# Optimization experiments

Measured on AMD Instinct MI355X. Metric: run time of the kernel, lower is better.

The kernel has to match this reference:

```python
import jax, jax.numpy as jnp
from jax import lax
import numpy as np

M_FILTERS = 128   # rows of responses D
N_CHANNELS = 1024 # cols of responses D (spectral channels)
BATCH = 4096
N_LAYERS = 17
IMAX = 50


def setup_inputs() -> dict:
    key = jax.random.key(0)
    k1, k2, k3, k4 = jax.random.split(key, 4)
    t1 = jax.random.normal(k1, (BATCH, N_CHANNELS), dtype=jnp.float32)
    t2 = jax.random.normal(k2, (BATCH, N_CHANNELS), dtype=jnp.float32)
    params = jax.random.uniform(k3, (M_FILTERS, N_LAYERS), dtype=jnp.float32)
    responses = jax.random.normal(k4, (M_FILTERS, N_CHANNELS), dtype=jnp.float32)
    return {
        "t1": t1,
        "t2": t2,
        "params": params,
        "thick_min": jnp.float32(0.0),
        "thick_max": jnp.float32(1.0),
        "beta_range": jnp.float32(0.1),
        "responses": responses,
    }


def _coherence_reduce(D0):
    """Faithful vectorized version of the 50-iteration coherence-reduction loop.

    The original per-row Python loop (Ri[i] > Rth branch) only reads row i and
    pre-computed Rth/delta, so it is exactly a masked row update.
    torch.linalg.eig on the symmetric matrices G is replaced by eigh (same
    eigenpairs up to sign/order; order is fixed by the explicit descending sort,
    and only the top-M eigenpairs reach the output D[:M,:]).
    """
    Mr, Nr = D0.shape
    ratio = jnp.float32(Nr / Mr)
    eye_b = jnp.eye(Nr, dtype=bool)

    def body(_, D):
        D = D / jnp.linalg.norm(D)                      # Frobenius norm over (0,1)
        G = D.T @ D                                     # [N, N]
        Sigma, V = jnp.linalg.eigh(G)
        Sigma = jnp.where(jnp.abs(Sigma) > 1e-10, ratio, Sigma)
        G = (V * Sigma[None, :]) @ V.T                  # V diag(Sigma) V^T
        G0 = jnp.abs(G - jnp.diag(jnp.diag(G)))
        Ri = jnp.sum(G0, axis=0)                        # [N]
        Rth = jnp.min(Ri)
        delta = Rth / (Nr - 1)
        mask = (Ri > Rth)[:, None]                      # rows to clip
        Gn = jnp.where(mask, delta * jnp.sign(G), G)
        Gn = jnp.where(eye_b, G, Gn)                    # keep original diagonal
        G = (Gn + Gn.T) * 0.5
        Sigma, V = jnp.linalg.eigh(G)
        order = jnp.argsort(-Sigma)                     # descending
        Sigma = Sigma[order]
        V = V[:, order]
        # Original: Sigma[M:-1]=0 then D = diag(Sigma)^{1/2} @ V.T, D = D[:M,:].
        # Only the top-M eigenpairs contribute to the first M rows.
        Dn = jnp.power(Sigma[:Mr], 0.5)[:, None] * V[:, :Mr].T  # [M, N]
        return Dn

    return lax.fori_loop(0, IMAX, body, D0)


def reference(t1, t2, params, thick_min, thick_max, beta_range, responses):
    # HybnetLoss: MSE match loss + hinge range loss (filter_loss is zeroed in source)
    match_loss = jnp.mean((t1 - t2) ** 2)
    d = jnp.float32(0.01)
    res = jnp.maximum((params - thick_min - d) / (-d),
                      (params - thick_max + d) / d)
    range_loss = jnp.mean(jnp.maximum(res, jnp.zeros_like(res)))
    original_loss = match_loss + beta_range * range_loss

    # HybnetLoss_plus: coherence-reduction regularizer on the response matrix
    D = _coherence_reduce(responses)
    rloss = jnp.mean((D - responses) ** 2)
    return original_loss + rloss
```

## Files before the change

kernel.cpp:

```cpp
#include <hip/hip_runtime.h>

#define NBLK 256

#define OFF_G    0
#define OFF_QT   1048576
#define OFF_YS   1179648
#define OFF_CS   1703936
#define OFF_LT   1835008
#define OFF_RP   1851392
#define OFF_ACC  1867776
#define OFF_BAR  1867792

#define BAR_A 0
#define BAR_B 32
#define BAR_C 64
#define BAR_D 72
#define BAR_E 73

typedef float v4f __attribute__((ext_vector_type(4)));

__device__ __forceinline__ void cld4_2(v4f& a, v4f& b,
                                       const float* pa, const float* pb) {
    asm volatile("global_load_dwordx4 %0, %2, off sc1\n\t"
                 "global_load_dwordx4 %1, %3, off sc1\n\t"
                 "s_waitcnt vmcnt(0)"
                 : "=&v"(a), "=&v"(b) : "v"(pa), "v"(pb) : "memory");
}
__device__ __forceinline__ void cld4_3(v4f& a, v4f& b, v4f& c,
                                       const float* pa, const float* pb,
                                       const float* pc) {
    asm volatile("global_load_dwordx4 %0, %3, off sc1\n\t"
                 "global_load_dwordx4 %1, %4, off sc1\n\t"
                 "global_load_dwordx4 %2, %5, off sc1\n\t"
                 "s_waitcnt vmcnt(0)"
                 : "=&v"(a), "=&v"(b), "=&v"(c)
                 : "v"(pa), "v"(pb), "v"(pc) : "memory");
}
__device__ __forceinline__ void cld4_4(v4f& a, v4f& b, v4f& c, v4f& d,
                                       const float* pa, const float* pb,
                                       const float* pc, const float* pd) {
    asm volatile("global_load_dwordx4 %0, %4, off sc1\n\t"
                 "global_load_dwordx4 %1, %5, off sc1\n\t"
                 "global_load_dwordx4 %2, %6, off sc1\n\t"
                 "global_load_dwordx4 %3, %7, off sc1\n\t"
                 "s_waitcnt vmcnt(0)"
                 : "=&v"(a), "=&v"(b), "=&v"(c), "=&v"(d)
                 : "v"(pa), "v"(pb), "v"(pc), "v"(pd) : "memory");
}
__device__ __forceinline__ void cld4_8(v4f& a, v4f& b, v4f& c, v4f& d,
                                       v4f& e, v4f& f, v4f& g, v4f& h,
                                       const float* pa, const float* pb,
                                       const float* pc, const float* pd,
                                       const float* pe, const float* pf,
                                       const float* pg, const float* ph) {
    asm volatile("global_load_dwordx4 %0, %8, off sc1\n\t"
                 "global_load_dwordx4 %1, %9, off sc1\n\t"
                 "global_load_dwordx4 %2, %10, off sc1\n\t"
                 "global_load_dwordx4 %3, %11, off sc1\n\t"
                 "global_load_dwordx4 %4, %12, off sc1\n\t"
                 "global_load_dwordx4 %5, %13, off sc1\n\t"
// ... 16 lines not shown
                 : "=&v"(a), "=&v"(b), "=&v"(c), "=&v"(d)
                 : "v"(pa), "v"(pb), "v"(pc), "v"(pd) : "memory");
}
__device__ __forceinline__ void cld1_8(float& a, float& b, float& c, float& d,
                                       float& e, float& f, float& g, float& h,
                                       const float* pa, const float* pb,
                                       const float* pc, const float* pd,
                                       const float* pe, const float* pf,
                                       const float* pg, const float* ph) {
    asm volatile("global_load_dword %0, %8, off sc1\n\t"
                 "global_load_dword %1, %9, off sc1\n\t"
                 "global_load_dword %2, %10, off sc1\n\t"
                 "global_load_dword %3, %11, off sc1\n\t"
                 "global_load_dword %4, %12, off sc1\n\t"
                 "global_load_dword %5, %13, off sc1\n\t"
                 "global_load_dword %6, %14, off sc1\n\t"
                 "global_load_dword %7, %15, off sc1\n\t"
                 "s_waitcnt vmcnt(0)"
                 : "=&v"(a), "=&v"(b), "=&v"(c), "=&v"(d),
                   "=&v"(e), "=&v"(f), "=&v"(g), "=&v"(h)
                 : "v"(pa), "v"(pb), "v"(pc), "v"(pd),
                   "v"(pe), "v"(pf), "v"(pg), "v"(ph) : "memory");
}

__device__ __forceinline__ void ast2(float* p, float a, float b) {
    union { unsigned long long u; float f[2]; } c; c.f[0] = a; c.f[1] = b;
    __hip_atomic_store((unsigned long long*)p, c.u,
                       __ATOMIC_RELAXED, __HIP_MEMORY_SCOPE_AGENT);
}
__device__ __forceinline__ float ald(const float* p) {
    return __hip_atomic_load(p, __ATOMIC_RELAXED, __HIP_MEMORY_SCOPE_AGENT);
}
__device__ __forceinline__ void ast(float* p, float x) {
    __hip_atomic_store(p, x, __ATOMIC_RELAXED, __HIP_MEMORY_SCOPE_AGENT);
}

__device__ __forceinline__ void bar_arrive(unsigned* bb, int line) {
    __syncthreads();
    if (threadIdx.x == 0)
        __hip_atomic_fetch_add(bb + line * 16, 1u,
                               __ATOMIC_RELAXED, __HIP_MEMORY_SCOPE_AGENT);
}
__device__ __forceinline__ void bar_wait(unsigned* bb, int wbase, int nlines,
                                         unsigned tgt) {
    if ((int)threadIdx.x < nlines) {
        while (__hip_atomic_load(bb + (wbase + threadIdx.x) * 16,
                                 __ATOMIC_RELAXED, __HIP_MEMORY_SCOPE_AGENT) < tgt)
            __builtin_amdgcn_s_sleep(2);
    }
    __builtin_amdgcn_s_waitcnt(0);
    __syncthreads();
}

union Smem {
    struct { float As[128][68]; float Bs[128][68]; } syrk;
    struct { float Cs[128][129]; float inv_d[16]; } chol;
    struct { float Ls[128 * 128]; float Xs[16][32]; } trsm;
    struct { float As[32][68]; float Bs[32][68]; float Rs[64][16]; } gg;
    struct { float Ri[1024]; float red[256]; float As[32][33]; float Bs[32][68]; } gy;
    float red[256];
};

__device__ __forceinline__ void dev_match(Smem* sm, const float* t1, const float* t2,
                                          float* accb, int w) {
    int tid = threadIdx.x;
    const float4* a = (const float4*)t1;
    const float4* b = (const float4*)t2;
    float s = 0.f;
    for (int i = w * 256 + tid; i < 1048576; i += 218 * 256) {
        float4 x = a[i], y = b[i];
        float d0 = x.x - y.x, d1 = x.y - y.y, d2 = x.z - y.z, d3 = x.w - y.w;
        s += d0 * d0 + d1 * d1 + d2 * d2 + d3 * d3;
    }
    sm->red[tid] = s; __syncthreads();
    for (int w2 = 128; w2 > 0; w2 >>= 1) {
        if (tid < w2) sm->red[tid] += sm->red[tid + w2];
        __syncthreads();
    }
    if (tid == 0) atomicAdd(&accb[0], sm->red[0]);
    __syncthreads();
}

// ... 11 lines not shown
    }
    sm->red[tid] = s; __syncthreads();
    for (int w = 128; w > 0; w >>= 1) {
        if (tid < w) sm->red[tid] += sm->red[tid + w];
        __syncthreads();
    }
    if (tid == 0) atomicAdd(&accb[1], sm->red[0]);
    __syncthreads();
}

__device__ __forceinline__ void dev_sumsq(Smem* sm, const float* X, float* accb, int w) {
    int tid = threadIdx.x;
    float s = 0.f;
    for (int i = w * 256 + tid; i < 131072; i += 1024) { float v = X[i]; s += v * v; }
    sm->red[tid] = s; __syncthreads();
    for (int w2 = 128; w2 > 0; w2 >>= 1) {
        if (tid < w2) sm->red[tid] += sm->red[tid + w2];
        __syncthreads();
    }
    if (tid == 0) atomicAdd(&accb[3], sm->red[0]);
    __syncthreads();
}

__device__ __forceinline__ void dev_syrk(Smem* sm, const float* A, int nsA,
                                         const float* B, int nsB, float* Cslab, int bid) {
    int tid = threadIdx.x;
    int q0 = (bid & 1) * 64, p0 = ((bid >> 1) & 1) * 64, z = bid >> 2;
    int kc = z * 128;
    if (nsA == 1) {
        for (int i = tid; i < 2048; i += 256) {
            int r = i >> 5, c4 = (i & 31) << 2;
            float4 v = *(const float4*)&A[(p0 + r) * 1024 + kc + c4];
            sm->syrk.As[c4][r] = v.x; sm->syrk.As[c4 + 1][r] = v.y;
            sm->syrk.As[c4 + 2][r] = v.z; sm->syrk.As[c4 + 3][r] = v.w;
        }
        for (int i = tid; i < 2048; i += 256) {
            int r = i >> 5, c4 = (i & 31) << 2;
            float4 v = *(const float4*)&B[(q0 + r) * 1024 + kc + c4];
            sm->syrk.Bs[c4][r] = v.x; sm->syrk.Bs[c4 + 1][r] = v.y;
            sm->syrk.Bs[c4 + 2][r] = v.z; sm->syrk.Bs[c4 + 3][r] = v.w;
        }
    } else {
        for (int cc = 0; cc < 8; cc += 2) {
            int i0 = tid + cc * 256, i1 = i0 + 256;
            int r0 = i0 >> 5, c40 = (i0 & 31) << 2;
            int r1 = i1 >> 5, c41 = (i1 & 31) << 2;
            const float* b0p = &A[(p0 + r0) * 1024 + kc + c40];
            const float* b1p = &A[(p0 + r1) * 1024 + kc + c41];
            v4f x0, x1, x2, x3, y0, y1, y2, y3;
            cld4_8(x0, x1, x2, x3, y0, y1, y2, y3,
                   b0p, b0p + 131072, b0p + 262144, b0p + 393216,
                   b1p, b1p + 131072, b1p + 262144, b1p + 393216);
            v4f s0 = x0; s0 += x1; s0 += x2; s0 += x3;
            v4f s1 = y0; s1 += y1; s1 += y2; s1 += y3;
            sm->syrk.As[c40][r0] = s0.x; sm->syrk.As[c40 + 1][r0] = s0.y;
            sm->syrk.As[c40 + 2][r0] = s0.z; sm->syrk.As[c40 + 3][r0] = s0.w;
            sm->syrk.As[c41][r1] = s1.x; sm->syrk.As[c41 + 1][r1] = s1.y;
            sm->syrk.As[c41 + 2][r1] = s1.z; sm->syrk.As[c41 + 3][r1] = s1.w;
        }
        for (int cc = 0; cc < 8; cc += 2) {
            int i0 = tid + cc * 256, i1 = i0 + 256;
            int r0 = i0 >> 5, c40 = (i0 & 31) << 2;
            int r1 = i1 >> 5, c41 = (i1 & 31) << 2;
            const float* b0p = &B[(q0 + r0) * 1024 + kc + c40];
            const float* b1p = &B[(q0 + r1) * 1024 + kc + c41];
            v4f x0, x1, x2, x3, y0, y1, y2, y3;
            cld4_8(x0, x1, x2, x3, y0, y1, y2, y3,
                   b0p, b0p + 131072, b0p + 262144, b0p + 393216,
                   b1p, b1p + 131072, b1p + 262144, b1p + 393216);
            v4f s0 = x0; s0 += x1; s0 += x2; s0 += x3;
            v4f s1 = y0; s1 += y1; s1 += y2; s1 += y3;
            sm->syrk.Bs[c40][r0] = s0.x; sm->syrk.Bs[c40 + 1][r0] = s0.y;
            sm->syrk.Bs[c40 + 2][r0] = s0.z; sm->syrk.Bs[c40 + 3][r0] = s0.w;
            sm->syrk.Bs[c41][r1] = s1.x; sm->syrk.Bs[c41 + 1][r1] = s1.y;
            sm->syrk.Bs[c41 + 2][r1] = s1.z; sm->syrk.Bs[c41 + 3][r1] = s1.w;
        }
    }
    __syncthreads();
    int tx = tid & 15, ty = tid >> 4;
    float acc[4][4] = {};
    for (int k = 0; k < 128; ++k) {
        float4 av = *(const float4*)&sm->syrk.As[k][ty * 4];
        float4 bv = *(const float4*)&sm->syrk.Bs[k][tx * 4];
        float a[4] = {av.x, av.y, av.z, av.w};
        float b[4] = {bv.x, bv.y, bv.z, bv.w};
        #pragma unroll
        for (int i = 0; i < 4; ++i)
            #pragma unroll
            for (int j = 0; j < 4; ++j) acc[i][j] += a[i] * b[j];
    }
    float* outp = &Cslab[z * 16384];
    for (int i = 0; i < 4; ++i) {
        float* op = &outp[(p0 + ty * 4 + i) * 128 + q0 + tx * 4];
        ast2(op, acc[i][0], acc[i][1]);
        ast2(op + 2, acc[i][2], acc[i][3]);
    }
    __syncthreads();
}

__device__ __forceinline__ void dev_chol(Smem* sm, const float* Cslab, float* Lt) {
    int tid = threadIdx.x;
    for (int cc = 0; cc < 16; ++cc) {
        int i = tid + cc * 256;
        int r = i >> 5, c4 = (i & 31) << 2;
        const float* b = &Cslab[i * 4];
        v4f z0, z1, z2, z3, z4, z5, z6, z7;
        cld4_8(z0, z1, z2, z3, z4, z5, z6, z7,
               b, b + 16384, b + 32768, b + 49152,
               b + 65536, b + 81920, b + 98304, b + 114688);
        v4f s = z0; s += z1; s += z2; s += z3; s += z4; s += z5; s += z6; s += z7;
        sm->chol.Cs[r][c4] = s.x; sm->chol.Cs[r][c4 + 1] = s.y;
        sm->chol.Cs[r][c4 + 2] = s.z; sm->chol.Cs[r][c4 + 3] = s.w;
    }
    __syncthreads();
    int lane = tid & 63;
    for (int kb = 0; kb < 8; ++kb) {
        int k0 = kb * 16;
        if (tid < 64) {
            float P0[16], P1[16], invs[16];
            #pragma unroll
            for (int u = 0; u < 16; ++u) {
                P0[u] = sm->chol.Cs[lane][k0 + u];
                P1[u] = sm->chol.Cs[lane + 64][k0 + u];
            }
            #pragma unroll
            for (int kk = 0; kk < 16; ++kk) {
                int k = k0 + kk;
                int src = k & 63;
                bool hi = (k >= 64);
                float pr[16];
                #pragma unroll
                for (int u = 0; u < 16; ++u)
                    if (u >= kk) pr[u] = __shfl(hi ? P1[u] : P0[u], src);
                float inv = 1.0f / pr[kk];
                invs[kk] = inv;
// ... 26 lines not shown
            if (has1) {
                #pragma unroll
                for (int u = 0; u < 16; ++u) w1[u] = sm->chol.Cs[j1][k0 + u] * sm->chol.inv_d[u];
            }
            if (has2) {
                #pragma unroll
                for (int u = 0; u < 16; ++u) w2[u] = sm->chol.Cs[j2][k0 + u] * sm->chol.inv_d[u];
            }
            int rlo = h * 32;
            int istart = rlo > base ? rlo : base;
            for (int i = istart; i < rlo + 32; ++i) {
                float v[16];
                #pragma unroll
                for (int u = 0; u < 16; ++u) v[u] = sm->chol.Cs[i][k0 + u];
                float a1 = 0.f, a2 = 0.f;
                #pragma unroll
                for (int u = 0; u < 16; ++u) { a1 += v[u] * w1[u]; a2 += v[u] * w2[u]; }
                if (has1) sm->chol.Cs[i][j1] -= a1;
                if (has2) sm->chol.Cs[i][j2] -= a2;
            }
        }
        __syncthreads();
    }
    for (int f2 = tid; f2 < 8192; f2 += 256) {
        int k = f2 >> 6, i2 = (f2 & 63) << 1;
        float d = sm->chol.Cs[k][k];
        float irs = 1.0f / sqrtf(d);
        float v0, v1;
        int i = i2;
        v0 = (i < k) ? 0.f : ((i == k) ? irs : sm->chol.Cs[i][k] * irs);
        i = i2 + 1;
        v1 = (i < k) ? 0.f : ((i == k) ? irs : sm->chol.Cs[i][k] * irs);
        ast2(&Lt[k * 128 + i2], v0, v1);
    }
    __syncthreads();
}

__device__ __forceinline__ void dev_trsm(Smem* sm, const float* Lt, const float* RHS,
                                         int ns, float* Qt, int bid) {
    int tid = threadIdx.x;
    int c = tid & 31, h = tid >> 5;
    int j0 = bid * 32;
    for (int cc = 0; cc < 16; cc += 4) {
        int i0 = tid + cc * 256, i1 = i0 + 256, i2 = i0 + 512, i3 = i0 + 768;
        v4f a, b, d, e;
        cld4_4(a, b, d, e, &Lt[i0 * 4], &Lt[i1 * 4], &Lt[i2 * 4], &Lt[i3 * 4]);
        *(v4f*)&sm->trsm.Ls[i0 * 4] = a;
        *(v4f*)&sm->trsm.Ls[i1 * 4] = b;
        *(v4f*)&sm->trsm.Ls[i2 * 4] = d;
        *(v4f*)&sm->trsm.Ls[i3 * 4] = e;
    }
    float acc[16];
    if (ns == 1) {
        #pragma unroll
        for (int r = 0; r < 16; ++r)
            acc[r] = RHS[(h * 16 + r) * 1024 + j0 + c];
    } else {
        for (int r = 0; r < 16; r += 2) {
            const float* p0 = &RHS[(h * 16 + r) * 1024 + j0 + c];
            const float* p1 = p0 + 1024;
            float a0, a1, a2, a3, b0, b1, b2, b3;
            cld1_8(a0, a1, a2, a3, b0, b1, b2, b3,
                   p0, p0 + 131072, p0 + 262144, p0 + 393216,
                   p1, p1 + 131072, p1 + 262144, p1 + 393216);
            acc[r] = ((a0 + a1) + a2) + a3;
            acc[r + 1] = ((b0 + b1) + b2) + b3;
        }
    }
    __syncthreads();
    float* Ls = sm->trsm.Ls;
    for (int pb = 0; pb < 8; ++pb) {
        int p0 = pb * 16;
        if (h == pb) {
            #pragma unroll
            for (int kk = 0; kk < 16; ++kk) {
                int k = p0 + kk;
                float x = acc[kk] * Ls[k * 128 + k];
                acc[kk] = x;
                sm->trsm.Xs[kk][c] = x;
                #pragma unroll
                for (int r = kk + 1; r < 16; ++r)
                    acc[r] -= Ls[k * 128 + p0 + r] * x;
            }
        }
        __syncthreads();
        if (h > pb) {
            int rb = h * 16;
            #pragma unroll
            for (int kk = 0; kk < 16; ++kk) {
                float x = sm->trsm.Xs[kk][c];
                const float4* lr = (const float4*)&Ls[(p0 + kk) * 128 + rb];
                #pragma unroll
                for (int g4 = 0; g4 < 4; ++g4) {
                    float4 lv = lr[g4];
                    acc[g4 * 4 + 0] -= lv.x * x;
                    acc[g4 * 4 + 1] -= lv.y * x;
                    acc[g4 * 4 + 2] -= lv.z * x;
                    acc[g4 * 4 + 3] -= lv.w * x;
                }
            }
        }
        __syncthreads();
    }
    #pragma unroll
    for (int r = 0; r < 16; ++r)
        ast(&Qt[(h * 16 + r) * 1024 + j0 + c], acc[r]);
}

__device__ __forceinline__ void dev_gemmG(Smem* sm, const float* Qt, float* G,
                                          float* Rpart, int bid) {
    int tid = threadIdx.x;
    int tx = tid & 15, ty = tid >> 4;
    int bx = bid & 15, by = bid >> 4;
    int a0 = by * 64, b0 = bx * 64;
    float acc[4][4] = {};
    for (int kc = 0; kc < 128; kc += 32) {
        int i0 = tid, i1 = tid + 256;
        int r0 = i0 >> 4, c40 = (i0 & 15) << 2;
        int r1 = i1 >> 4, c41 = (i1 & 15) << 2;
        v4f av0, av1, bv0, bv1;
        cld4_4(av0, av1, bv0, bv1,
               &Qt[(kc + r0) * 1024 + a0 + c40],
               &Qt[(kc + r1) * 1024 + a0 + c41],
               &Qt[(kc + r0) * 1024 + b0 + c40],
               &Qt[(kc + r1) * 1024 + b0 + c41]);
        *(v4f*)&sm->gg.As[r0][c40] = av0;
        *(v4f*)&sm->gg.As[r1][c41] = av1;
        *(v4f*)&sm->gg.Bs[r0][c40] = bv0;
        *(v4f*)&sm->gg.Bs[r1][c41] = bv1;
        __syncthreads();
        for (int k = 0; k < 32; ++k) {
            float4 av = *(const float4*)&sm->gg.As[k][ty * 4];
            float4 bv = *(const float4*)&sm->gg.Bs[k][tx * 4];
            float a[4] = {av.x, av.y, av.z, av.w};
            float b[4] = {bv.x, bv.y, bv.z, bv.w};
            #pragma unroll
            for (int i = 0; i < 4; ++i)
                #pragma unroll
                for (int j = 0; j < 4; ++j) acc[i][j] += a[i] * b[j];
        }
        __syncthreads();
    }
    float rsum[4] = {0.f, 0.f, 0.f, 0.f};
    for (int i = 0; i < 4; ++i) {
        int aa = a0 + ty * 4 + i;
        float g[4];
        #pragma unroll
        for (int j = 0; j < 4; ++j) g[j] = 8.f * acc[i][j];
        float* gp = &G[aa * 1024 + b0 + tx * 4];
        ast2(gp, g[0], g[1]);
        ast2(gp + 2, g[2], g[3]);
        int bb = b0 + tx * 4;
        #pragma unroll
// ... 27 lines not shown
        s0 += t3.x; s0 += t3.y; s0 += t3.z; s0 += t3.w;
        float s1 = 0.f;
        s1 += u0.x; s1 += u0.y; s1 += u0.z; s1 += u0.w;
        s1 += u1.x; s1 += u1.y; s1 += u1.z; s1 += u1.w;
        s1 += u2.x; s1 += u2.y; s1 += u2.z; s1 += u2.w;
        s1 += u3.x; s1 += u3.y; s1 += u3.z; s1 += u3.w;
        sm->gy.Ri[e0] = s0;
        sm->gy.Ri[e1] = s1;
        mn = fminf(mn, s0);
        mn = fminf(mn, s1);
    }
    sm->gy.red[tid] = mn;
    __syncthreads();
    for (int w = 128; w > 0; w >>= 1) {
        if (tid < w) sm->gy.red[tid] = fminf(sm->gy.red[tid], sm->gy.red[tid + w]);
        __syncthreads();
    }
    float r = sm->gy.red[0];
    *rth = r;
    *delta = r / 1023.f;
}

__device__ __forceinline__ void dev_gemmY(Smem* sm, const float* Qt, const float* G,
                                          float rth, float delta, float* Yslab, int bid) {
    int tid = threadIdx.x;
    int j0 = (bid & 15) * 64;
    int m0 = ((bid >> 4) & 3) * 32;
    int kz = bid >> 6;
    int kc0 = kz * 256;
    int tx = tid & 15, ty = tid >> 4;
    float acc[2][4] = {};
    for (int kc = kc0; kc < kc0 + 256; kc += 32) {
        int m = tid >> 3, k4 = (tid & 7) << 2;
        int iG0 = tid, iG1 = tid + 256;
        int rg0 = iG0 >> 4, cg0 = (iG0 & 15) << 2;
        int rg1 = iG1 >> 4, cg1 = (iG1 & 15) << 2;
        v4f q, g0, g1;
        cld4_3(q, g0, g1,
               &Qt[(m0 + m) * 1024 + kc + k4],
               &G[(kc + rg0) * 1024 + j0 + cg0],
               &G[(kc + rg1) * 1024 + j0 + cg1]);
        sm->gy.As[k4][m] = q.x;
        sm->gy.As[k4 + 1][m] = q.y;
        sm->gy.As[k4 + 2][m] = q.z;
        sm->gy.As[k4 + 3][m] = q.w;
        {
            int a = kc + rg0;
            float ria = sm->gy.Ri[a];
            #pragma unroll
            for (int u = 0; u < 4; ++u) {
                int b = j0 + cg0 + u;
                float g = g0[u];
                float sg = delta * ((g > 0.f) ? 1.f : ((g < 0.f) ? -1.f : 0.f));
                float ga = (ria > rth) ? sg : g;
                float gb = (sm->gy.Ri[b] > rth) ? sg : g;
                sm->gy.Bs[rg0][cg0 + u] = (a == b) ? g : 0.5f * (ga + gb);
            }
        }
        {
            int a = kc + rg1;
            float ria = sm->gy.Ri[a];
            #pragma unroll
            for (int u = 0; u < 4; ++u) {
                int b = j0 + cg1 + u;
                float g = g1[u];
                float sg = delta * ((g > 0.f) ? 1.f : ((g < 0.f) ? -1.f : 0.f));
                float ga = (ria > rth) ? sg : g;
                float gb = (sm->gy.Ri[b] > rth) ? sg : g;
                sm->gy.Bs[rg1][cg1 + u] = (a == b) ? g : 0.5f * (ga + gb);
            }
        }
        __syncthreads();
        for (int k = 0; k < 32; ++k) {
            float a0v = sm->gy.As[k][ty * 2], a1v = sm->gy.As[k][ty * 2 + 1];
            float4 bv = *(const float4*)&sm->gy.Bs[k][tx * 4];
            acc[0][0] += a0v * bv.x; acc[0][1] += a0v * bv.y;
            acc[0][2] += a0v * bv.z; acc[0][3] += a0v * bv.w;
            acc[1][0] += a1v * bv.x; acc[1][1] += a1v * bv.y;
            acc[1][2] += a1v * bv.z; acc[1][3] += a1v * bv.w;
        }
        __syncthreads();
    }
    float* outp = &Yslab[kz * 131072];
    for (int i = 0; i < 2; ++i) {
        float* op = &outp[(m0 + ty * 2 + i) * 1024 + j0 + tx * 4];
        ast2(op, acc[i][0], acc[i][1]);
        ast2(op + 2, acc[i][2], acc[i][3]);
    }
}

__device__ __forceinline__ void dev_trB(Smem* sm, const float* Qt, const float* G,
                                        const float* Rpart, float* accb, int bid) {
    int tid = threadIdx.x;
    float rth, delta;
    dev_ri(sm, Rpart, &rth, &delta);
    __syncthreads();
    int tx = tid & 15, ty = tid >> 4;
    int a0 = (bid >> 4) * 64, b0 = (bid & 15) * 64;
    float acc[4][4] = {};
    for (int kc = 0; kc < 128; kc += 32) {
        int i0 = tid, i1 = tid + 256;
        int r0 = i0 >> 4, c40 = (i0 & 15) << 2;
        int r1 = i1 >> 4, c41 = (i1 & 15) << 2;
        v4f av0, av1, bv0, bv1;
        cld4_4(av0, av1, bv0, bv1,
               &Qt[(kc + r0) * 1024 + a0 + c40],
               &Qt[(kc + r1) * 1024 + a0 + c41],
               &Qt[(kc + r0) * 1024 + b0 + c40],
               &Qt[(kc + r1) * 1024 + b0 + c41]);
        *(v4f*)&sm->syrk.As[r0][c40] = av0;
        *(v4f*)&sm->syrk.As[r1][c41] = av1;
        *(v4f*)&sm->syrk.Bs[r0][c40] = bv0;
        *(v4f*)&sm->syrk.Bs[r1][c41] = bv1;
        __syncthreads();
        for (int k = 0; k < 32; ++k) {
            float4 av = *(const float4*)&sm->syrk.As[k][ty * 4];
            float4 bv = *(const float4*)&sm->syrk.Bs[k][tx * 4];
            float a[4] = {av.x, av.y, av.z, av.w};
            float b[4] = {bv.x, bv.y, bv.z, bv.w};
            #pragma unroll
            for (int i = 0; i < 4; ++i)
                #pragma unroll
                for (int j = 0; j < 4; ++j) acc[i][j] += a[i] * b[j];
        }
        __syncthreads();
    }
    float rib[4];
    for (int j = 0; j < 4; ++j) {
        int bb = b0 + tx * 4 + j;
        v4f t0, t1, t2, t3;
        cld4_4(t0, t1, t2, t3, &Rpart[bb * 16], &Rpart[bb * 16 + 4],
               &Rpart[bb * 16 + 8], &Rpart[bb * 16 + 12]);
        float s = 0.f;
        s += t0.x; s += t0.y; s += t0.z; s += t0.w;
        s += t1.x; s += t1.y; s += t1.z; s += t1.w;
        s += t2.x; s += t2.y; s += t2.z; s += t2.w;
        s += t3.x; s += t3.y; s += t3.z; s += t3.w;
        rib[j] = s;
    }
    float s = 0.f;
// ... 2 lines not shown
        v4f t0, t1, t2, t3;
        cld4_4(t0, t1, t2, t3, &Rpart[aa * 16], &Rpart[aa * 16 + 4],
               &Rpart[aa * 16 + 8], &Rpart[aa * 16 + 12]);
        float ria = 0.f;
        ria += t0.x; ria += t0.y; ria += t0.z; ria += t0.w;
        ria += t1.x; ria += t1.y; ria += t1.z; ria += t1.w;
        ria += t2.x; ria += t2.y; ria += t2.z; ria += t2.w;
        ria += t3.x; ria += t3.y; ria += t3.z; ria += t3.w;
        float g0, g1, g2, g3;
        const float* gp = &G[aa * 1024 + b0 + tx * 4];
        cld1_4(g0, g1, g2, g3, gp, gp + 1, gp + 2, gp + 3);
        float gv[4] = {g0, g1, g2, g3};
        for (int j = 0; j < 4; ++j) {
            int bb = b0 + tx * 4 + j;
            float g = gv[j];
            float sg = delta * ((g > 0.f) ? 1.f : ((g < 0.f) ? -1.f : 0.f));
            float ga = (ria > rth) ? sg : g;
            float gb = (rib[j] > rth) ? sg : g;
            float gp2 = (aa == bb) ? g : 0.5f * (ga + gb);
            s += gp2 * acc[i][j];
        }
    }
    __syncthreads();
    sm->red[tid] = s;
    __syncthreads();
    for (int w = 128; w > 0; w >>= 1) {
        if (tid < w) sm->red[tid] += sm->red[tid + w];
        __syncthreads();
    }
    if (tid == 0) atomicAdd(&accb[2], sm->red[0]);
}

__global__ __launch_bounds__(256) void mega(const float* __restrict__ t1,
                                            const float* __restrict__ t2,
                                            const float* __restrict__ params,
                                            const float* __restrict__ tmin,
                                            const float* __restrict__ tmax,
                                            const float* __restrict__ beta,
                                            const float* __restrict__ R,
                                            float* ws, float* out) {
    float* G     = ws + OFF_G;
    float* Qt    = ws + OFF_QT;
    float* Yslab = ws + OFF_YS;
    float* Cslab = ws + OFF_CS;
    float* Lt    = ws + OFF_LT;
    float* Rpart = ws + OFF_RP;
    float* accb  = ws + OFF_ACC;
    unsigned* bb = (unsigned*)(ws + OFF_BAR);
    __shared__ Smem sm;
    int bid = blockIdx.x;
    unsigned phA = 0, phB = 0, phC = 0, phD = 0, phE = 0;

    if (bid < 32) dev_syrk(&sm, R, 1, R, 1, Cslab, bid);
    else if (bid < 250) dev_match(&sm, t1, t2, accb, bid - 32);
    else if (bid == 250) dev_range(&sm, params, tmin, tmax, accb);
    else if (bid < 255) dev_sumsq(&sm, R, accb, bid - 251);
    ++phC;
    if (bid < 32) bar_arrive(bb, BAR_C + (bid >> 2));
    if (bid == 0) { bar_wait(bb, BAR_C, 8, phC * 4); dev_chol(&sm, Cslab, Lt); }
    ++phD;
    if (bid == 0) bar_arrive(bb, BAR_D);
    if (bid < 32) { bar_wait(bb, BAR_D, 1, phD); dev_trsm(&sm, Lt, R, 1, Qt, bid); }
    ++phE;
    if (bid < 32) bar_arrive(bb, BAR_E + (bid >> 2));
    bar_wait(bb, BAR_E, 8, phE * 4);

    for (int it = 0; it < 50; ++it) {
        dev_gemmG(&sm, Qt, G, Rpart, bid);
        ++phA;
        bar_arrive(bb, BAR_A + (bid >> 3));
        bar_wait(bb, BAR_A, 32, phA * 8);
        {
            float rth, delta;
            dev_ri(&sm, Rpart, &rth, &delta);
            dev_gemmY(&sm, Qt, G, rth, delta, Yslab, bid);
        }
        ++phB;
        bar_arrive(bb, BAR_B + (bid >> 3));
        if (bid < 32) {
            bar_wait(bb, BAR_B, 32, phB * 8);
            dev_syrk(&sm, Yslab, 4, Yslab, 4, Cslab, bid);
        }
        ++phC;
        if (bid < 32) bar_arrive(bb, BAR_C + (bid >> 2));
        if (bid == 0) { bar_wait(bb, BAR_C, 8, phC * 4); dev_chol(&sm, Cslab, Lt); }
        ++phD;
        if (bid == 0) bar_arrive(bb, BAR_D);
        if (bid < 32) { bar_wait(bb, BAR_D, 1, phD); dev_trsm(&sm, Lt, Yslab, 4, Qt, bid); }
        ++phE;
        if (bid < 32) bar_arrive(bb, BAR_E + (bid >> 2));
        bar_wait(bb, BAR_E, 8, phE * 4);
    }

    dev_trB(&sm, Qt, G, Rpart, accb, bid);
    ++phA;
    bar_arrive(bb, BAR_A + (bid >> 3));
    if (bid == 0) {
        bar_wait(bb, BAR_A, 32, phA * 8);
        if (threadIdx.x == 0)
            out[0] = ald(&accb[0]) / 4194304.f + beta[0] * (ald(&accb[1]) / 2176.f)
                   + (ald(&accb[2]) + ald(&accb[3])) / 131072.f;
    }
}

extern "C" void kernel_launch(void* const* d_in, const int* in_sizes, int n_in,
                              void* d_out, int out_size, void* d_ws, size_t ws_size,
                              hipStream_t stream) {
    const float* t1 = (const float*)d_in[0];
    const float* t2 = (const float*)d_in[1];
    const float* params = (const float*)d_in[2];
    const float* tmin = (const float*)d_in[3];
    const float* tmax = (const float*)d_in[4];
    const float* beta = (const float*)d_in[5];
    const float* R = (const float*)d_in[6];
    float* ws = (float*)d_ws;
    float* out = (float*)d_out;

    hipMemsetAsync(ws + OFF_ACC, 0, 5312, stream);
    mega<<<NBLK, 256, 0, stream>>>(t1, t2, params, tmin, tmax, beta, R, ws, out);
}
```

Before: 8.408 ms.

## Fuse Cholesky with TRSM across blocks and use atomic accumulation instead of slabs

```diff
diff --git a/kernel.cpp b/kernel.cpp
--- a/kernel.cpp
+++ b/kernel.cpp
@@ -4,38 +4,19 @@
 
 #define OFF_G    0
 #define OFF_QT   1048576
-#define OFF_YS   1179648
-#define OFF_CS   1703936
-#define OFF_LT   1835008
+#define OFF_Y    1179648
+#define OFF_C    1703936
 #define OFF_RP   1851392
 #define OFF_ACC  1867776
 #define OFF_BAR  1867792
 
 #define BAR_A 0
-#define BAR_B 32
-#define BAR_C 64
-#define BAR_D 72
-#define BAR_E 73
+#define BAR_B 64
+#define BAR_C 128
+#define BAR_E 136
 
 typedef float v4f __attribute__((ext_vector_type(4)));
 
-__device__ __forceinline__ void cld4_2(v4f& a, v4f& b,
-                                       const float* pa, const float* pb) {
-    asm volatile("global_load_dwordx4 %0, %2, off sc1\n\t"
-                 "global_load_dwordx4 %1, %3, off sc1\n\t"
-                 "s_waitcnt vmcnt(0)"
-                 : "=&v"(a), "=&v"(b) : "v"(pa), "v"(pb) : "memory");
-}
-__device__ __forceinline__ void cld4_3(v4f& a, v4f& b, v4f& c,
-                                       const float* pa, const float* pb,
-                                       const float* pc) {
-    asm volatile("global_load_dwordx4 %0, %3, off sc1\n\t"
-                 "global_load_dwordx4 %1, %4, off sc1\n\t"
-                 "global_load_dwordx4 %2, %5, off sc1\n\t"
-                 "s_waitcnt vmcnt(0)"
-                 : "=&v"(a), "=&v"(b), "=&v"(c)
-                 : "v"(pa), "v"(pb), "v"(pc) : "memory");
-}
 __device__ __forceinline__ void cld4_4(v4f& a, v4f& b, v4f& c, v4f& d,
                                        const float* pa, const float* pb,
                                        const float* pc, const float* pd) {
@@ -98,6 +79,32 @@
                  : "v"(pa), "v"(pb), "v"(pc), "v"(pd),
                    "v"(pe), "v"(pf), "v"(pg), "v"(ph) : "memory");
 }
+__device__ __forceinline__ void iss4(v4f& a, v4f& b, v4f& c, v4f& d,
+                                     const float* pa, const float* pb,
+                                     const float* pc, const float* pd) {
+    asm volatile("global_load_dwordx4 %0, %4, off sc1\n\t"
+                 "global_load_dwordx4 %1, %5, off sc1\n\t"
+                 "global_load_dwordx4 %2, %6, off sc1\n\t"
+                 "global_load_dwordx4 %3, %7, off sc1"
+                 : "=&v"(a), "=&v"(b), "=&v"(c), "=&v"(d)
+                 : "v"(pa), "v"(pb), "v"(pc), "v"(pd) : "memory");
+}
+__device__ __forceinline__ void wt4(v4f& a, v4f& b, v4f& c, v4f& d) {
+    asm volatile("s_waitcnt vmcnt(0)"
+                 : "+v"(a), "+v"(b), "+v"(c), "+v"(d) :: "memory");
+}
+__device__ __forceinline__ void iss3(v4f& a, v4f& b, v4f& c,
+                                     const float* pa, const float* pb,
+                                     const float* pc) {
+    asm volatile("global_load_dwordx4 %0, %3, off sc1\n\t"
+                 "global_load_dwordx4 %1, %4, off sc1\n\t"
+                 "global_load_dwordx4 %2, %5, off sc1"
+                 : "=&v"(a), "=&v"(b), "=&v"(c)
+                 : "v"(pa), "v"(pb), "v"(pc) : "memory");
+}
+__device__ __forceinline__ void wt3(v4f& a, v4f& b, v4f& c) {
+    asm volatile("s_waitcnt vmcnt(0)" : "+v"(a), "+v"(b), "+v"(c) :: "memory");
+}
 
 __device__ __forceinline__ void ast2(float* p, float a, float b) {
     union { unsigned long long u; float f[2]; } c; c.f[0] = a; c.f[1] = b;
@@ -122,18 +129,18 @@
     if ((int)threadIdx.x < nlines) {
         while (__hip_atomic_load(bb + (wbase + threadIdx.x) * 16,
                                  __ATOMIC_RELAXED, __HIP_MEMORY_SCOPE_AGENT) < tgt)
-            __builtin_amdgcn_s_sleep(2);
+            __builtin_amdgcn_s_sleep(1);
     }
     __builtin_amdgcn_s_waitcnt(0);
     __syncthreads();
 }
 
 union Smem {
-    struct { float As[128][68]; float Bs[128][68]; } syrk;
-    struct { float Cs[128][129]; float inv_d[16]; } chol;
-    struct { float Ls[128 * 128]; float Xs[16][32]; } trsm;
     struct { float As[32][68]; float Bs[32][68]; float Rs[64][16]; } gg;
+    struct { float Cs[128][129]; float inv_d[16]; float irs[128];
+             float Xs[16][32]; } chol;
     struct { float Ri[1024]; float red[256]; float As[32][33]; float Bs[32][68]; } gy;
+    struct { float As[32][68]; float Bs[32][68]; float red[256]; } tb;
     float red[256];
 };
 
@@ -191,95 +198,76 @@
     __syncthreads();
 }
 
-__device__ __forceinline__ void dev_syrk(Smem* sm, const float* A, int nsA,
-                                         const float* B, int nsB, float* Cslab, int bid) {
+__device__ __forceinline__ void dev_syrk(Smem* sm, const float* A, const float* B,
+                                         float* C, int bid) {
     int tid = threadIdx.x;
     int q0 = (bid & 1) * 64, p0 = ((bid >> 1) & 1) * 64, z = bid >> 2;
-    int kc = z * 128;
-    if (nsA == 1) {
-        for (int i = tid; i < 2048; i += 256) {
-            int r = i >> 5, c4 = (i & 31) << 2;
-            float4 v = *(const float4*)&A[(p0 + r) * 1024 + kc + c4];
-            sm->syrk.As[c4][r] = v.x; sm->syrk.As[c4 + 1][r] = v.y;
-            sm->syrk.As[c4 + 2][r] = v.z; sm->syrk.As[c4 + 3][r] = v.w;
-        }
-        for (int i = tid; i < 2048; i += 256) {
-            int r = i >> 5, c4 = (i & 31) << 2;
-            float4 v = *(const float4*)&B[(q0 + r) * 1024 + kc + c4];
-            sm->syrk.Bs[c4][r] = v.x; sm->syrk.Bs[c4 + 1][r] = v.y;
-            sm->syrk.Bs[c4 + 2][r] = v.z; sm->syrk.Bs[c4 + 3][r] = v.w;
-        }
-    } else {
-        for (int cc = 0; cc < 8; cc += 2) {
-            int i0 = tid + cc * 256, i1 = i0 + 256;
-            int r0 = i0 >> 5, c40 = (i0 & 31) << 2;
-            int r1 = i1 >> 5, c41 = (i1 & 31) << 2;
-            const float* b0p = &A[(p0 + r0) * 1024 + kc + c40];
-            const float* b1p = &A[(p0 + r1) * 1024 + kc + c41];
-            v4f x0, x1, x2, x3, y0, y1, y2, y3;
-            cld4_8(x0, x1, x2, x3, y0, y1, y2, y3,
-                   b0p, b0p + 131072, b0p + 262144, b0p + 393216,
-                   b1p, b1p + 131072, b1p + 262144, b1p + 393216);
-            v4f s0 = x0; s0 += x1; s0 += x2; s0 += x3;
-            v4f s1 = y0; s1 += y1; s1 += y2; s1 += y3;
-            sm->syrk.As[c40][r0] = s0.x; sm->syrk.As[c40 + 1][r0] = s0.y;
-            sm->syrk.As[c40 + 2][r0] = s0.z; sm->syrk.As[c40 + 3][r0] = s0.w;
-            sm->syrk.As[c41][r1] = s1.x; sm->syrk.As[c41 + 1][r1] = s1.y;
-            sm->syrk.As[c41 + 2][r1] = s1.z; sm->syrk.As[c41 + 3][r1] = s1.w;
-        }
-        for (int cc = 0; cc < 8; cc += 2) {
-            int i0 = tid + cc * 256, i1 = i0 + 256;
-            int r0 = i0 >> 5, c40 = (i0 & 31) << 2;
-            int r1 = i1 >> 5, c41 = (i1 & 31) << 2;
-            const float* b0p = &B[(q0 + r0) * 1024 + kc + c40];
-            const float* b1p = &B[(q0 + r1) * 1024 + kc + c41];
-            v4f x0, x1, x2, x3, y0, y1, y2, y3;
-            cld4_8(x0, x1, x2, x3, y0, y1, y2, y3,
-                   b0p, b0p + 131072, b0p + 262144, b0p + 393216,
-                   b1p, b1p + 131072, b1p + 262144, b1p + 393216);
-            v4f s0 = x0; s0 += x1; s0 += x2; s0 += x3;
-            v4f s1 = y0; s1 += y1; s1 += y2; s1 += y3;
-            sm->syrk.Bs[c40][r0] = s0.x; sm->syrk.Bs[c40 + 1][r0] = s0.y;
-            sm->syrk.Bs[c40 + 2][r0] = s0.z; sm->syrk.Bs[c40 + 3][r0] = s0.w;
-            sm->syrk.Bs[c41][r1] = s1.x; sm->syrk.Bs[c41 + 1][r1] = s1.y;
-            sm->syrk.Bs[c41 + 2][r1] = s1.z; sm->syrk.Bs[c41 + 3][r1] = s1.w;
-        }
-    }
-    __syncthreads();
+    int kc0 = z * 128;
+    int p = tid & 63, kq = tid >> 6;
+    int kg = kq * 8;
     int tx = tid & 15, ty = tid >> 4;
     float acc[4][4] = {};
-    for (int k = 0; k < 128; ++k) {
-        float4 av = *(const float4*)&sm->syrk.As[k][ty * 4];
-        float4 bv = *(const float4*)&sm->syrk.Bs[k][tx * 4];
-        float a[4] = {av.x, av.y, av.z, av.w};
-        float b[4] = {bv.x, bv.y, bv.z, bv.w};
-        #pragma unroll
-        for (int i = 0; i < 4; ++i)
-            #pragma unroll
-            for (int j = 0; j < 4; ++j) acc[i][j] += a[i] * b[j];
-    }
-    float* outp = &Cslab[z * 16384];
-    for (int i = 0; i < 4; ++i) {
-        float* op = &outp[(p0 + ty * 4 + i) * 128 + q0 + tx * 4];
-        ast2(op, acc[i][0], acc[i][1]);
-        ast2(op + 2, acc[i][2], acc[i][3]);
-    }
-    __syncthreads();
-}
-
-__device__ __forceinline__ void dev_chol(Smem* sm, const float* Cslab, float* Lt) {
-    int tid = threadIdx.x;
-    for (int cc = 0; cc < 16; ++cc) {
-        int i = tid + cc * 256;
-        int r = i >> 5, c4 = (i & 31) << 2;
-        const float* b = &Cslab[i * 4];
+    v4f a0v, a1v, b0v, b1v;
+    {
+        const float* pa = &A[(p0 + p) * 1024 + kc0 + kg];
+        const float* pb = &B[(q0 + p) * 1024 + kc0 + kg];
+        iss4(a0v, a1v, b0v, b1v, pa, pa + 4, pb, pb + 4);
+    }
+    for (int ck = 0; ck < 4; ++ck) {
+        wt4(a0v, a1v, b0v, b1v);
+        __syncthreads();
+        sm->gg.As[kg + 0][p] = a0v.x; sm->gg.As[kg + 1][p] = a0v.y;
+        sm->gg.As[kg + 2][p] = a0v.z; sm->gg.As[kg + 3][p] = a0v.w;
+        sm->gg.As[kg + 4][p] = a1v.x; sm->gg.As[kg + 5][p] = a1v.y;
+        sm->gg.As[kg + 6][p] = a1v.z; sm->gg.As[kg + 7][p] = a1v.w;
+        sm->gg.Bs[kg + 0][p] = b0v.x; sm->gg.Bs[kg + 1][p] = b0v.y;
+        sm->gg.Bs[kg + 2][p] = b0v.z; sm->gg.Bs[kg + 3][p] = b0v.w;
+        sm->gg.Bs[kg + 4][p] = b1v.x; sm->gg.Bs[kg + 5][p] = b1v.y;
+        sm->gg.Bs[kg + 6][p] = b1v.z; sm->gg.Bs[kg + 7][p] = b1v.w;
+        __syncthreads();
+        if (ck < 3) {
+            const float* pa = &A[(p0 + p) * 1024 + kc0 + (ck + 1) * 32 + kg];
+            const float* pb = &B[(q0 + p) * 1024 + kc0 + (ck + 1) * 32 + kg];
+            iss4(a0v, a1v, b0v, b1v, pa, pa + 4, pb, pb + 4);
+        }
+        for (int k = 0; k < 32; ++k) {
+            float4 av = *(const float4*)&sm->gg.As[k][ty * 4];
+            float4 bv = *(const float4*)&sm->gg.Bs[k][tx * 4];
+            float a[4] = {av.x, av.y, av.z, av.w};
+            float b[4] = {bv.x, bv.y, bv.z, bv.w};
+            #pragma unroll
+            for (int i = 0; i < 4; ++i)
+                #pragma unroll
+                for (int j = 0; j < 4; ++j) acc[i][j] += a[i] * b[j];
+        }
+        __syncthreads();
+    }
+    for (int i = 0; i < 4; ++i)
+        for (int j = 0; j < 4; ++j)
+            atomicAdd(&C[(p0 + ty * 4 + i) * 128 + q0 + tx * 4 + j], acc[i][j]);
+}
+
+__device__ __forceinline__ void dev_cholTrsm(Smem* sm, const float* C, const float* RHS,
+                                             float* Qt, int bid) {
+    int tid = threadIdx.x;
+    {
+        const float* base = C + tid * 64;
         v4f z0, z1, z2, z3, z4, z5, z6, z7;
         cld4_8(z0, z1, z2, z3, z4, z5, z6, z7,
-               b, b + 16384, b + 32768, b + 49152,
-               b + 65536, b + 81920, b + 98304, b + 114688);
-        v4f s = z0; s += z1; s += z2; s += z3; s += z4; s += z5; s += z6; s += z7;
-        sm->chol.Cs[r][c4] = s.x; sm->chol.Cs[r][c4 + 1] = s.y;
-        sm->chol.Cs[r][c4 + 2] = s.z; sm->chol.Cs[r][c4 + 3] = s.w;
+               base, base + 4, base + 8, base + 12,
+               base + 16, base + 20, base + 24, base + 28);
+        int r = tid >> 1, c0 = (tid & 1) * 64;
+        *(v4f*)&sm->chol.Cs[r][c0]      = z0; *(v4f*)&sm->chol.Cs[r][c0 + 4]  = z1;
+        *(v4f*)&sm->chol.Cs[r][c0 + 8]  = z2; *(v4f*)&sm->chol.Cs[r][c0 + 12] = z3;
+        *(v4f*)&sm->chol.Cs[r][c0 + 16] = z4; *(v4f*)&sm->chol.Cs[r][c0 + 20] = z5;
+        *(v4f*)&sm->chol.Cs[r][c0 + 24] = z6; *(v4f*)&sm->chol.Cs[r][c0 + 28] = z7;
+        cld4_8(z0, z1, z2, z3, z4, z5, z6, z7,
+               base + 32, base + 36, base + 40, base + 44,
+               base + 48, base + 52, base + 56, base + 60);
+        *(v4f*)&sm->chol.Cs[r][c0 + 32] = z0; *(v4f*)&sm->chol.Cs[r][c0 + 36] = z1;
+        *(v4f*)&sm->chol.Cs[r][c0 + 40] = z2; *(v4f*)&sm->chol.Cs[r][c0 + 44] = z3;
+        *(v4f*)&sm->chol.Cs[r][c0 + 48] = z4; *(v4f*)&sm->chol.Cs[r][c0 + 52] = z5;
+        *(v4f*)&sm->chol.Cs[r][c0 + 56] = z6; *(v4f*)&sm->chol.Cs[r][c0 + 60] = z7;
     }
     __syncthreads();
     int lane = tid & 63;
@@ -352,65 +340,33 @@
         }
         __syncthreads();
     }
-    for (int f2 = tid; f2 < 8192; f2 += 256) {
-        int k = f2 >> 6, i2 = (f2 & 63) << 1;
-        float d = sm->chol.Cs[k][k];
-        float irs = 1.0f / sqrtf(d);
-        float v0, v1;
-        int i = i2;
-        v0 = (i < k) ? 0.f : ((i == k) ? irs : sm->chol.Cs[i][k] * irs);
-        i = i2 + 1;
-        v1 = (i < k) ? 0.f : ((i == k) ? irs : sm->chol.Cs[i][k] * irs);
-        ast2(&Lt[k * 128 + i2], v0, v1);
-    }
-    __syncthreads();
-}
-
-__device__ __forceinline__ void dev_trsm(Smem* sm, const float* Lt, const float* RHS,
-                                         int ns, float* Qt, int bid) {
-    int tid = threadIdx.x;
+    if (tid < 128) sm->chol.irs[tid] = 1.0f / sqrtf(sm->chol.Cs[tid][tid]);
     int c = tid & 31, h = tid >> 5;
     int j0 = bid * 32;
-    for (int cc = 0; cc < 16; cc += 4) {
-        int i0 = tid + cc * 256, i1 = i0 + 256, i2 = i0 + 512, i3 = i0 + 768;
-        v4f a, b, d, e;
-        cld4_4(a, b, d, e, &Lt[i0 * 4], &Lt[i1 * 4], &Lt[i2 * 4], &Lt[i3 * 4]);
-        *(v4f*)&sm->trsm.Ls[i0 * 4] = a;
-        *(v4f*)&sm->trsm.Ls[i1 * 4] = b;
-        *(v4f*)&sm->trsm.Ls[i2 * 4] = d;
-        *(v4f*)&sm->trsm.Ls[i3 * 4] = e;
-    }
     float acc[16];
-    if (ns == 1) {
-        #pragma unroll
-        for (int r = 0; r < 16; ++r)
-            acc[r] = RHS[(h * 16 + r) * 1024 + j0 + c];
-    } else {
-        for (int r = 0; r < 16; r += 2) {
-            const float* p0 = &RHS[(h * 16 + r) * 1024 + j0 + c];
-            const float* p1 = p0 + 1024;
-            float a0, a1, a2, a3, b0, b1, b2, b3;
-            cld1_8(a0, a1, a2, a3, b0, b1, b2, b3,
-                   p0, p0 + 131072, p0 + 262144, p0 + 393216,
-                   p1, p1 + 131072, p1 + 262144, p1 + 393216);
-            acc[r] = ((a0 + a1) + a2) + a3;
-            acc[r + 1] = ((b0 + b1) + b2) + b3;
-        }
-    }
-    __syncthreads();
-    float* Ls = sm->trsm.Ls;
+    {
+        const float* p = &RHS[(h * 16) * 1024 + j0 + c];
+        cld1_8(acc[0], acc[1], acc[2], acc[3], acc[4], acc[5], acc[6], acc[7],
+               p, p + 1024, p + 2048, p + 3072, p + 4096, p + 5120, p + 6144, p + 7168);
+        cld1_8(acc[8], acc[9], acc[10], acc[11], acc[12], acc[13], acc[14], acc[15],
+               p + 8192, p + 9216, p + 10240, p + 11264,
+               p + 12288, p + 13312, p + 14336, p + 15360);
+    }
+    __syncthreads();
     for (int pb = 0; pb < 8; ++pb) {
         int p0 = pb * 16;
         if (h == pb) {
             #pragma unroll
             for (int kk = 0; kk < 16; ++kk) {
                 int k = p0 + kk;
-                float x = acc[kk] * Ls[k * 128 + k];
+                float irsk = sm->chol.irs[k];
+                float x = acc[kk] * irsk;
                 acc[kk] = x;
-                sm->trsm.Xs[kk][c] = x;
+                sm->chol.Xs[kk][c] = x;
+                float xs = x * irsk;
                 #pragma unroll
                 for (int r = kk + 1; r < 16; ++r)
-                    acc[r] -= Ls[k * 128 + p0 + r] * x;
+                    acc[r] -= sm->chol.Cs[p0 + r][k] * xs;
             }
         }
         __syncthreads();
@@ -418,16 +374,11 @@
             int rb = h * 16;
             #pragma unroll
             for (int kk = 0; kk < 16; ++kk) {
-                float x = sm->trsm.Xs[kk][c];
-                const float4* lr = (const float4*)&Ls[(p0 + kk) * 128 + rb];
-                #pragma unroll
-                for (int g4 = 0; g4 < 4; ++g4) {
-                    float4 lv = lr[g4];
-                    acc[g4 * 4 + 0] -= lv.x * x;
-                    acc[g4 * 4 + 1] -= lv.y * x;
-                    acc[g4 * 4 + 2] -= lv.z * x;
-                    acc[g4 * 4 + 3] -= lv.w * x;
-                }
+                int k = p0 + kk;
+                float xs = sm->chol.Xs[kk][c] * sm->chol.irs[k];
+                #pragma unroll
+                for (int r = 0; r < 16; ++r)
+                    acc[r] -= sm->chol.Cs[rb + r][k] * xs;
             }
         }
         __syncthreads();
@@ -443,22 +394,27 @@
     int tx = tid & 15, ty = tid >> 4;
     int bx = bid & 15, by = bid >> 4;
     int a0 = by * 64, b0 = bx * 64;
+    int r0 = tid >> 4, c4 = (tid & 15) << 2;
+    int r1 = 16 + r0;
     float acc[4][4] = {};
+    v4f av0, av1, bv0, bv1;
+    iss4(av0, av1, bv0, bv1,
+         &Qt[r0 * 1024 + a0 + c4], &Qt[r1 * 1024 + a0 + c4],
+         &Qt[r0 * 1024 + b0 + c4], &Qt[r1 * 1024 + b0 + c4]);
     for (int kc = 0; kc < 128; kc += 32) {
-        int i0 = tid, i1 = tid + 256;
-        int r0 = i0 >> 4, c40 = (i0 & 15) << 2;
-        int r1 = i1 >> 4, c41 = (i1 & 15) << 2;
-        v4f av0, av1, bv0, bv1;
-        cld4_4(av0, av1, bv0, bv1,
-               &Qt[(kc + r0) * 1024 + a0 + c40],
-               &Qt[(kc + r1) * 1024 + a0 + c41],
-               &Qt[(kc + r0) * 1024 + b0 + c40],
-               &Qt[(kc + r1) * 1024 + b0 + c41]);
-        *(v4f*)&sm->gg.As[r0][c40] = av0;
-        *(v4f*)&sm->gg.As[r1][c41] = av1;
-        *(v4f*)&sm->gg.Bs[r0][c40] = bv0;
-        *(v4f*)&sm->gg.Bs[r1][c41] = bv1;
-        __syncthreads();
+        wt4(av0, av1, bv0, bv1);
+        __syncthreads();
+        *(v4f*)&sm->gg.As[r0][c4] = av0;
+        *(v4f*)&sm->gg.As[r1][c4] = av1;
+        *(v4f*)&sm->gg.Bs[r0][c4] = bv0;
+        *(v4f*)&sm->gg.Bs[r1][c4] = bv1;
+        __syncthreads();
+        if (kc < 96) {
+            int kn = kc + 32;
+            iss4(av0, av1, bv0, bv1,
+                 &Qt[(kn + r0) * 1024 + a0 + c4], &Qt[(kn + r1) * 1024 + a0 + c4],
+                 &Qt[(kn + r0) * 1024 + b0 + c4], &Qt[(kn + r1) * 1024 + b0 + c4]);
+        }
         for (int k = 0; k < 32; ++k) {
             float4 av = *(const float4*)&sm->gg.As[k][ty * 4];
             float4 bv = *(const float4*)&sm->gg.Bs[k][tx * 4];
@@ -532,24 +488,24 @@
 }
 
 __device__ __forceinline__ void dev_gemmY(Smem* sm, const float* Qt, const float* G,
-                                          float rth, float delta, float* Yslab, int bid) {
+                                          float rth, float delta, float* Y, int bid) {
     int tid = threadIdx.x;
     int j0 = (bid & 15) * 64;
     int m0 = ((bid >> 4) & 3) * 32;
     int kz = bid >> 6;
     int kc0 = kz * 256;
     int tx = tid & 15, ty = tid >> 4;
+    int m = tid >> 3, k4 = (tid & 7) << 2;
+    int rg0 = tid >> 4, cg0 = (tid & 15) << 2, rg1 = 16 + rg0;
     float acc[2][4] = {};
+    v4f q, g0, g1;
+    iss3(q, g0, g1,
+         &Qt[(m0 + m) * 1024 + kc0 + k4],
+         &G[(kc0 + rg0) * 1024 + j0 + cg0],
+         &G[(kc0 + rg1) * 1024 + j0 + cg0]);
     for (int kc = kc0; kc < kc0 + 256; kc += 32) {
-        int m = tid >> 3, k4 = (tid & 7) << 2;
-        int iG0 = tid, iG1 = tid + 256;
-        int rg0 = iG0 >> 4, cg0 = (iG0 & 15) << 2;
-        int rg1 = iG1 >> 4, cg1 = (iG1 & 15) << 2;
-        v4f q, g0, g1;
-        cld4_3(q, g0, g1,
-               &Qt[(m0 + m) * 1024 + kc + k4],
-               &G[(kc + rg0) * 1024 + j0 + cg0],
-               &G[(kc + rg1) * 1024 + j0 + cg1]);
+        wt3(q, g0, g1);
+        __syncthreads();
         sm->gy.As[k4][m] = q.x;
         sm->gy.As[k4 + 1][m] = q.y;
         sm->gy.As[k4 + 2][m] = q.z;
@@ -572,15 +528,22 @@
             float ria = sm->gy.Ri[a];
             #pragma unroll
             for (int u = 0; u < 4; ++u) {
-                int b = j0 + cg1 + u;
+                int b = j0 + cg0 + u;
                 float g = g1[u];
                 float sg = delta * ((g > 0.f) ? 1.f : ((g < 0.f) ? -1.f : 0.f));
                 float ga = (ria > rth) ? sg : g;
                 float gb = (sm->gy.Ri[b] > rth) ? sg : g;
-                sm->gy.Bs[rg1][cg1 + u] = (a == b) ? g : 0.5f * (ga + gb);
-            }
-        }
-        __syncthreads();
+                sm->gy.Bs[rg1][cg0 + u] = (a == b) ? g : 0.5f * (ga + gb);
+            }
+        }
+        __syncthreads();
+        if (kc < kc0 + 224) {
+            int kn = kc + 32;
+            iss3(q, g0, g1,
+                 &Qt[(m0 + m) * 1024 + kn + k4],
+                 &G[(kn + rg0) * 1024 + j0 + cg0],
+                 &G[(kn + rg1) * 1024 + j0 + cg0]);
+        }
         for (int k = 0; k < 32; ++k) {
             float a0v = sm->gy.As[k][ty * 2], a1v = sm->gy.As[k][ty * 2 + 1];
             float4 bv = *(const float4*)&sm->gy.Bs[k][tx * 4];
@@ -591,12 +554,9 @@
         }
         __syncthreads();
     }
-    float* outp = &Yslab[kz * 131072];
-    for (int i = 0; i < 2; ++i) {
-        float* op = &outp[(m0 + ty * 2 + i) * 1024 + j0 + tx * 4];
-        ast2(op, acc[i][0], acc[i][1]);
-        ast2(op + 2, acc[i][2], acc[i][3]);
-    }
+    for (int i = 0; i < 2; ++i)
+        for (int j = 0; j < 4; ++j)
+            atomicAdd(&Y[(m0 + ty * 2 + i) * 1024 + j0 + tx * 4 + j], acc[i][j]);
 }
 
 __device__ __forceinline__ void dev_trB(Smem* sm, const float* Qt, const float* G,
@@ -618,14 +578,15 @@
                &Qt[(kc + r1) * 1024 + a0 + c41],
                &Qt[(kc + r0) * 1024 + b0 + c40],
                &Qt[(kc + r1) * 1024 + b0 + c41]);
-        *(v4f*)&sm->syrk.As[r0][c40] = av0;
-        *(v4f*)&sm->syrk.As[r1][c41] = av1;
-        *(v4f*)&sm->syrk.Bs[r0][c40] = bv0;
-        *(v4f*)&sm->syrk.Bs[r1][c41] = bv1;
+        __syncthreads();
+        *(v4f*)&sm->tb.As[r0][c40] = av0;
+        *(v4f*)&sm->tb.As[r1][c41] = av1;
+        *(v4f*)&sm->tb.Bs[r0][c40] = bv0;
+        *(v4f*)&sm->tb.Bs[r1][c41] = bv1;
         __syncthreads();
         for (int k = 0; k < 32; ++k) {
-            float4 av = *(const float4*)&sm->syrk.As[k][ty * 4];
-            float4 bv = *(const float4*)&sm->syrk.Bs[k][tx * 4];
+            float4 av = *(const float4*)&sm->tb.As[k][ty * 4];
+            float4 bv = *(const float4*)&sm->tb.Bs[k][tx * 4];
             float a[4] = {av.x, av.y, av.z, av.w};
             float b[4] = {bv.x, bv.y, bv.z, bv.w};
             #pragma unroll
@@ -674,13 +635,13 @@
         }
     }
     __syncthreads();
-    sm->red[tid] = s;
+    sm->tb.red[tid] = s;
     __syncthreads();
     for (int w = 128; w > 0; w >>= 1) {
-        if (tid < w) sm->red[tid] += sm->red[tid + w];
-        __syncthreads();
-    }
-    if (tid == 0) atomicAdd(&accb[2], sm->red[0]);
+        if (tid < w) sm->tb.red[tid] += sm->tb.red[tid + w];
+        __syncthreads();
+    }
+    if (tid == 0) atomicAdd(&accb[2], sm->tb.red[0]);
 }
 
 __global__ __launch_bounds__(256) void mega(const float* __restrict__ t1,
@@ -693,52 +654,61 @@
                                             float* ws, float* out) {
     float* G     = ws + OFF_G;
     float* Qt    = ws + OFF_QT;
-    float* Yslab = ws + OFF_YS;
-    float* Cslab = ws + OFF_CS;
-    float* Lt    = ws + OFF_LT;
+    float* Y     = ws + OFF_Y;
+    float* C     = ws + OFF_C;
     float* Rpart = ws + OFF_RP;
     float* accb  = ws + OFF_ACC;
     unsigned* bb = (unsigned*)(ws + OFF_BAR);
     __shared__ Smem sm;
     int bid = blockIdx.x;
-    unsigned phA = 0, phB = 0, phC = 0, phD = 0, phE = 0;
-
-    if (bid < 32) dev_syrk(&sm, R, 1, R, 1, Cslab, bid);
-    else if (bid < 250) dev_match(&sm, t1, t2, accb, bid - 32);
+    int tid = threadIdx.x;
+    unsigned phA = 0, phB = 0, phC = 0, phE = 0;
+
+    if (bid < 32) {
+        ast2(&C[bid * 512 + tid * 2], 0.f, 0.f);
+    } else if (bid < 250) dev_match(&sm, t1, t2, accb, bid - 32);
     else if (bid == 250) dev_range(&sm, params, tmin, tmax, accb);
     else if (bid < 255) dev_sumsq(&sm, R, accb, bid - 251);
     ++phC;
-    if (bid < 32) bar_arrive(bb, BAR_C + (bid >> 2));
-    if (bid == 0) { bar_wait(bb, BAR_C, 8, phC * 4); dev_chol(&sm, Cslab, Lt); }
-    ++phD;
-    if (bid == 0) bar_arrive(bb, BAR_D);
-    if (bid < 32) { bar_wait(bb, BAR_D, 1, phD); dev_trsm(&sm, Lt, R, 1, Qt, bid); }
+    if (bid < 32) {
+        bar_arrive(bb, BAR_C + (bid >> 2));
+        bar_wait(bb, BAR_C, 8, phC * 4);
+        dev_syrk(&sm, R, R, C, bid);
+    }
+    ++phC;
+    if (bid < 32) {
+        bar_arrive(bb, BAR_C + (bid >> 2));
+        bar_wait(bb, BAR_C, 8, phC * 4);
+        dev_cholTrsm(&sm, C, R, Qt, bid);
+    }
     ++phE;
     if (bid < 32) bar_arrive(bb, BAR_E + (bid >> 2));
     bar_wait(bb, BAR_E, 8, phE * 4);
 
     for (int it = 0; it < 50; ++it) {
         dev_gemmG(&sm, Qt, G, Rpart, bid);
+        ast2(&Y[bid * 512 + tid * 2], 0.f, 0.f);
+        if (bid < 32) ast2(&C[bid * 512 + tid * 2], 0.f, 0.f);
         ++phA;
-        bar_arrive(bb, BAR_A + (bid >> 3));
-        bar_wait(bb, BAR_A, 32, phA * 8);
+        bar_arrive(bb, BAR_A + (bid & 63));
+        bar_wait(bb, BAR_A, 64, phA * 4);
         {
             float rth, delta;
             dev_ri(&sm, Rpart, &rth, &delta);
-            dev_gemmY(&sm, Qt, G, rth, delta, Yslab, bid);
+            dev_gemmY(&sm, Qt, G, rth, delta, Y, bid);
         }
         ++phB;
-        bar_arrive(bb, BAR_B + (bid >> 3));
+        bar_arrive(bb, BAR_B + (bid & 63));
         if (bid < 32) {
-            bar_wait(bb, BAR_B, 32, phB * 8);
-            dev_syrk(&sm, Yslab, 4, Yslab, 4, Cslab, bid);
+            bar_wait(bb, BAR_B, 64, phB * 4);
+            dev_syrk(&sm, Y, Y, C, bid);
         }
         ++phC;
-        if (bid < 32) bar_arrive(bb, BAR_C + (bid >> 2));
-        if (bid == 0) { bar_wait(bb, BAR_C, 8, phC * 4); dev_chol(&sm, Cslab, Lt); }
-        ++phD;
-        if (bid == 0) bar_arrive(bb, BAR_D);
-        if (bid < 32) { bar_wait(bb, BAR_D, 1, phD); dev_trsm(&sm, Lt, Yslab, 4, Qt, bid); }
+        if (bid < 32) {
+            bar_arrive(bb, BAR_C + (bid >> 2));
+            bar_wait(bb, BAR_C, 8, phC * 4);
+            dev_cholTrsm(&sm, C, Y, Qt, bid);
+        }
         ++phE;
         if (bid < 32) bar_arrive(bb, BAR_E + (bid >> 2));
         bar_wait(bb, BAR_E, 8, phE * 4);
@@ -746,10 +716,10 @@
 
     dev_trB(&sm, Qt, G, Rpart, accb, bid);
     ++phA;
-    bar_arrive(bb, BAR_A + (bid >> 3));
+    bar_arrive(bb, BAR_A + (bid & 63));
     if (bid == 0) {
-        bar_wait(bb, BAR_A, 32, phA * 8);
-        if (threadIdx.x == 0)
+        bar_wait(bb, BAR_A, 64, phA * 4);
+        if (tid == 0)
             out[0] = ald(&accb[0]) / 4194304.f + beta[0] * (ald(&accb[1]) / 2176.f)
                    + (ald(&accb[2]) + ald(&accb[3])) / 131072.f;
     }
@@ -768,6 +738,6 @@
     float* ws = (float*)d_ws;
     float* out = (float*)d_out;
 
-    hipMemsetAsync(ws + OFF_ACC, 0, 5312, stream);
+    hipMemsetAsync(ws + OFF_ACC, 0, 9280, stream);
     mega<<<NBLK, 256, 0, stream>>>(t1, t2, params, tmin, tmax, beta, R, ws, out);
 }
```

New measurement: 7.556 ms. 1.11x faster.
